# Optimization experiments

Hardware: AMD Instinct MI355X
Metric: run time of the kernel (lower is better)

Reference implementation:

```python
import jax, jax.numpy as jnp
import numpy as np

KD, KY, KX = 3, 3, 3  # kernel_size from init_kwargs


def setup_inputs() -> dict:
    key = jax.random.key(0)
    x = jax.random.normal(key, (4, 2, 64, 256, 256), dtype=jnp.float32)
    return {"x": x}


def reference(x):
    # x: [B, CH, D, H, W]
    B, CH, D, H, W = x.shape
    pd, py, px = (KD - 1) // 2, (KY - 1) // 2, (KX - 1) // 2
    # replicate padding (torch F.pad mode='replicate' == jnp.pad mode='edge')
    xp = jnp.pad(x, ((0, 0), (0, 0), (pd, pd), (py, py), (px, px)), mode='edge')
    center = (KD * KY * KX) // 2  # flattened center position, excluded from max
    # running max over the 26 non-center neighbors; never materializes the
    # [B, CH, 27, D, H, W] tensor the torch conv3d path creates.
    max_nc = jnp.full(x.shape, -jnp.inf, dtype=x.dtype)
    idx = 0
    for i in range(KD):
        for j in range(KY):
            for k in range(KX):
                if idx != center:
                    shifted = xp[:, :, i:i + D, j:j + H, k:k + W]
                    max_nc = jnp.maximum(max_nc, shifted)
                idx += 1
    mask = x > max_nc  # strict local maximum (excluding self)
    return x * mask.astype(x.dtype)
```

## Files before the change

kernel.cpp:

```cpp
#include <hip/hip_runtime.h>


constexpr int D_   = 64;
constexpr int H_   = 256;
constexpr int W_   = 256;
constexpr int HW_  = H_ * W_;
constexpr int NVOL = 8;
constexpr int DC   = 16;
constexpr int RY   = 8;
constexpr int RS   = RY + 2;
constexpr int NBUF = 4;
constexpr int S    = DC + 2;

__device__ __forceinline__ float f3(float a, float b, float c) {
    return fmaxf(fmaxf(a, b), c);
}

__device__ __forceinline__ void gload16(const float* g, float* l) {
    __builtin_amdgcn_global_load_lds(
        (const __attribute__((address_space(1))) void*)g,
        (__attribute__((address_space(3))) void*)l,
        16, 0, 0);
}

__device__ __forceinline__ void vmwait(int n) {
    switch (n) {
    case 0: asm volatile("s_waitcnt vmcnt(0)" ::: "memory"); break;
    case 1: asm volatile("s_waitcnt vmcnt(1)" ::: "memory"); break;
    case 2: asm volatile("s_waitcnt vmcnt(2)" ::: "memory"); break;
    case 3: asm volatile("s_waitcnt vmcnt(3)" ::: "memory"); break;
    case 4: asm volatile("s_waitcnt vmcnt(4)" ::: "memory"); break;
    case 5: asm volatile("s_waitcnt vmcnt(5)" ::: "memory"); break;
    case 6: asm volatile("s_waitcnt vmcnt(6)" ::: "memory"); break;
    default: asm volatile("s_waitcnt vmcnt(0)" ::: "memory"); break;
    }
}

__global__ __launch_bounds__(512, 8)
void nms3d(const float* __restrict__ x, float* __restrict__ out)
{
    __shared__ float lds[NBUF][RS * W_];

    const int tx = threadIdx.x;
    const int ty = threadIdx.y;

    const int bid  = blockIdx.x;
    const int n    = bid & 7;
    const int rest = bid >> 3;
    const int z0   = (rest & 3) * DC;
    const int h0   = (rest >> 2) * RY;
    const int h    = h0 + ty;
    const int c    = tx << 2;

    const float* __restrict__ base  = x   + (size_t)n * D_ * HW_;
    float* __restrict__       obase = out + (size_t)n * D_ * HW_;

    const int grA = min(max(h0 - 1 + ty, 0), H_ - 1);
    const int grB = min(max(h0 - 1 + RY + ty, 0), H_ - 1);
    const float* gA = base + (size_t)grA * W_ + c;
    const float* gB = base + (size_t)grB * W_ + c;

    auto stage = [&](int t) {
        const int zc = min(max(z0 - 1 + t, 0), D_ - 1);
        const size_t zo = (size_t)zc * HW_;
        float* lp = &lds[t & (NBUF - 1)][0];
        gload16(gA + zo, lp + ty * W_);
        if (ty < 2) gload16(gB + zo, lp + (RY + ty) * W_);
    };

    stage(0);
    stage(1);

    float4 vm9_pp = {0,0,0,0};
    float4 vm9_p  = {0,0,0,0};
    float4 cr8_p  = {0,0,0,0};
    float4 vprev  = {0,0,0,0};

#pragma unroll
    for (int t = 0; t < S; ++t) {
        if (t + 2 < S) stage(t + 2);

        int nhi, nlo;
        if      (t <= 2)     { nhi = 2; nlo = 4; }
        else if (t == 3)     { nhi = 3; nlo = 5; }
        else if (t <= S - 3) { nhi = 4; nlo = 6; }
        else if (t == S - 2) { nhi = 3; nlo = 4; }
        else                 { nhi = 2; nlo = 2; }
        vmwait(ty < 2 ? nlo : nhi);

        __builtin_amdgcn_s_barrier();
        asm volatile("" ::: "memory");

        const float* p = &lds[t & (NBUF - 1)][0];
        const float4 a0 = *(const float4*)(p + (ty    ) * W_ + c);
        const float4 b0 = *(const float4*)(p + (ty + 1) * W_ + c);
        const float4 d0 = *(const float4*)(p + (ty + 2) * W_ + c);

        float4 va;
        va.x = fmaxf(a0.x, d0.x); va.y = fmaxf(a0.y, d0.y);
        va.z = fmaxf(a0.z, d0.z); va.w = fmaxf(a0.w, d0.w);

        float vaL = __shfl_up(va.w, 1);   if (tx == 0)  vaL = va.x;
        float vaR = __shfl_down(va.x, 1); if (tx == 63) vaR = va.w;
        float bL  = __shfl_up(b0.w, 1);   if (tx == 0)  bL  = b0.x;
        float bR  = __shfl_down(b0.x, 1); if (tx == 63) bR  = b0.w;

        float4 hv, nb;
        hv.x = f3(vaL, va.x, va.y);  hv.y = f3(va.x, va.y, va.z);
        hv.z = f3(va.y, va.z, va.w); hv.w = f3(va.z, va.w, vaR);
        nb.x = fmaxf(bL,  b0.y);  nb.y = fmaxf(b0.x, b0.z);
        nb.z = fmaxf(b0.y, b0.w); nb.w = fmaxf(b0.z, bR);

        float4 c8, cur;
        c8.x  = fmaxf(hv.x, nb.x); c8.y  = fmaxf(hv.y, nb.y);
        c8.z  = fmaxf(hv.z, nb.z); c8.w  = fmaxf(hv.w, nb.w);
        cur.x = fmaxf(c8.x, b0.x); cur.y = fmaxf(c8.y, b0.y);
        cur.z = fmaxf(c8.z, b0.z); cur.w = fmaxf(c8.w, b0.w);

        if (t >= 2) {
            const int zi = z0 - 1 + t;
            float4 mx, o;
            mx.x = f3(vm9_pp.x, cr8_p.x, cur.x);
            mx.y = f3(vm9_pp.y, cr8_p.y, cur.y);
            mx.z = f3(vm9_pp.z, cr8_p.z, cur.z);
            mx.w = f3(vm9_pp.w, cr8_p.w, cur.w);
            o.x = vprev.x > mx.x ? vprev.x : 0.0f;
            o.y = vprev.y > mx.y ? vprev.y : 0.0f;
            o.z = vprev.z > mx.z ? vprev.z : 0.0f;
            o.w = vprev.w > mx.w ? vprev.w : 0.0f;
            *(float4*)(obase + (size_t)(zi - 1) * HW_ + (size_t)h * W_ + c) = o;
        }
        vm9_pp = vm9_p; vm9_p = cur; cr8_p = c8; vprev = b0;
    }
}

extern "C" void kernel_launch(void* const* d_in, const int* in_sizes, int n_in,
                              void* d_out, int out_size, void* d_ws, size_t ws_size,
                              hipStream_t stream)
{
    const float* x = (const float*)d_in[0];
    float* out = (float*)d_out;
    dim3 block(64, RY, 1);
    dim3 grid(NVOL * (D_ / DC) * (H_ / RY), 1, 1);
    nms3d<<<grid, block, 0, stream>>>(x, out);
}
```

Baseline: 239.4 us.

## Deepen LDS prefetch to three slices and use nontemporal output stores

Raises the async global-to-LDS prefetch distance from two to three depth slices, using five LDS ring buffers with modulo indexing and recomputed vmcnt wait thresholds. The aim is to keep more loads in flight and hide memory latency. Output stores become nontemporal so streaming writes do not pollute cache. The larger LDS footprint lowers the occupancy hint from 8 to 6, which may reduce latency hiding across blocks.

```diff
diff --git a/kernel.cpp b/kernel.cpp
--- a/kernel.cpp
+++ b/kernel.cpp
@@ -9,8 +9,11 @@
 constexpr int DC   = 16;
 constexpr int RY   = 8;
 constexpr int RS   = RY + 2;
-constexpr int NBUF = 4;
+constexpr int NBUF = 5;
 constexpr int S    = DC + 2;
+constexpr int PF   = 3;
+
+typedef float f32x4 __attribute__((ext_vector_type(4)));
 
 __device__ __forceinline__ float f3(float a, float b, float c) {
     return fmaxf(fmaxf(a, b), c);
@@ -32,11 +35,33 @@
     case 4: asm volatile("s_waitcnt vmcnt(4)" ::: "memory"); break;
     case 5: asm volatile("s_waitcnt vmcnt(5)" ::: "memory"); break;
     case 6: asm volatile("s_waitcnt vmcnt(6)" ::: "memory"); break;
+    case 7: asm volatile("s_waitcnt vmcnt(7)" ::: "memory"); break;
+    case 8: asm volatile("s_waitcnt vmcnt(8)" ::: "memory"); break;
+    case 9: asm volatile("s_waitcnt vmcnt(9)" ::: "memory"); break;
     default: asm volatile("s_waitcnt vmcnt(0)" ::: "memory"); break;
     }
 }
 
-__global__ __launch_bounds__(512, 8)
+__device__ __forceinline__ constexpr int wait_lo(int t) {
+    if (t <= 2)      return 6;
+    if (t == 3)      return 7;
+    if (t == 4)      return 8;
+    if (t <= S - 4)  return 9;
+    if (t == S - 3)  return 7;
+    if (t == S - 2)  return 5;
+    return 3;
+}
+__device__ __forceinline__ constexpr int wait_hi(int t) {
+    if (t <= 2)      return 3;
+    if (t == 3)      return 4;
+    if (t == 4)      return 5;
+    if (t <= S - 4)  return 6;
+    if (t == S - 3)  return 5;
+    if (t == S - 2)  return 4;
+    return 3;
+}
+
+__global__ __launch_bounds__(512, 6)
 void nms3d(const float* __restrict__ x, float* __restrict__ out)
 {
     __shared__ float lds[NBUF][RS * W_];
@@ -63,13 +88,14 @@
     auto stage = [&](int t) {
         const int zc = min(max(z0 - 1 + t, 0), D_ - 1);
         const size_t zo = (size_t)zc * HW_;
-        float* lp = &lds[t & (NBUF - 1)][0];
+        float* lp = &lds[t % NBUF][0];
         gload16(gA + zo, lp + ty * W_);
         if (ty < 2) gload16(gB + zo, lp + (RY + ty) * W_);
     };
 
     stage(0);
     stage(1);
+    stage(2);
 
     float4 vm9_pp = {0,0,0,0};
     float4 vm9_p  = {0,0,0,0};
@@ -78,20 +104,13 @@
 
 #pragma unroll
     for (int t = 0; t < S; ++t) {
-        if (t + 2 < S) stage(t + 2);
+        if (t + PF < S) stage(t + PF);
 
-        int nhi, nlo;
-        if      (t <= 2)     { nhi = 2; nlo = 4; }
-        else if (t == 3)     { nhi = 3; nlo = 5; }
-        else if (t <= S - 3) { nhi = 4; nlo = 6; }
-        else if (t == S - 2) { nhi = 3; nlo = 4; }
-        else                 { nhi = 2; nlo = 2; }
-        vmwait(ty < 2 ? nlo : nhi);
-
+        vmwait(ty < 2 ? wait_lo(t) : wait_hi(t));
         __builtin_amdgcn_s_barrier();
         asm volatile("" ::: "memory");
 
-        const float* p = &lds[t & (NBUF - 1)][0];
+        const float* p = &lds[t % NBUF][0];
         const float4 a0 = *(const float4*)(p + (ty    ) * W_ + c);
         const float4 b0 = *(const float4*)(p + (ty + 1) * W_ + c);
         const float4 d0 = *(const float4*)(p + (ty + 2) * W_ + c);
@@ -119,16 +138,19 @@
 
         if (t >= 2) {
             const int zi = z0 - 1 + t;
-            float4 mx, o;
+            float4 mx;
             mx.x = f3(vm9_pp.x, cr8_p.x, cur.x);
             mx.y = f3(vm9_pp.y, cr8_p.y, cur.y);
             mx.z = f3(vm9_pp.z, cr8_p.z, cur.z);
             mx.w = f3(vm9_pp.w, cr8_p.w, cur.w);
+            f32x4 o;
             o.x = vprev.x > mx.x ? vprev.x : 0.0f;
             o.y = vprev.y > mx.y ? vprev.y : 0.0f;
             o.z = vprev.z > mx.z ? vprev.z : 0.0f;
             o.w = vprev.w > mx.w ? vprev.w : 0.0f;
-            *(float4*)(obase + (size_t)(zi - 1) * HW_ + (size_t)h * W_ + c) = o;
+            f32x4* dst = (f32x4*)(obase + (size_t)(zi - 1) * HW_ +
+                                  (size_t)h * W_ + c);
+            __builtin_nontemporal_store(o, dst);
         }
         vm9_pp = vm9_p; vm9_p = cur; cr8_p = c8; vprev = b0;
     }
```

After: 238.7 us. Within noise of the previous version (-0.3%).
